# Optimization experiments

Measured on AMD Instinct MI355X. Metric: run time of the kernel, lower is better.

The kernel has to match this reference:

```python
import jax, jax.numpy as jnp
import numpy as np

N_NODES = 100000
N_EDGES = 600000
NODE_IN = 387
HID = 128
EDGE_DIM = 7


def _p(key, shape, scale=0.02):
    return jax.random.normal(key, shape, dtype=jnp.float32) * scale


def setup_inputs() -> dict:
    key = jax.random.key(0)
    ks = jax.random.split(key, 24)
    x = jax.random.normal(ks[0], (N_NODES, NODE_IN), dtype=jnp.float32)
    edge_index = jax.random.randint(ks[1], (2, N_EDGES), 0, N_NODES, dtype=jnp.int64)
    edge_attr = jax.random.normal(ks[2], (N_EDGES, EDGE_DIM), dtype=jnp.float32)
    return {
        "x": x,
        "edge_index": edge_index,
        "edge_attr": edge_attr,
        # conv1: edge lin (7 -> 387), mlp (387 -> 128 -> 128)
        "e1_w": _p(ks[3], (EDGE_DIM, NODE_IN)), "e1_b": jnp.zeros((NODE_IN,), jnp.float32),
        "m1_w1": _p(ks[4], (NODE_IN, HID)), "m1_b1": jnp.zeros((HID,), jnp.float32),
        "m1_w2": _p(ks[5], (HID, HID)), "m1_b2": jnp.zeros((HID,), jnp.float32),
        # conv2: edge lin (7 -> 128), mlp (128 -> 128 -> 128)
        "e2_w": _p(ks[6], (EDGE_DIM, HID)), "e2_b": jnp.zeros((HID,), jnp.float32),
        "m2_w1": _p(ks[7], (HID, HID)), "m2_b1": jnp.zeros((HID,), jnp.float32),
        "m2_w2": _p(ks[8], (HID, HID)), "m2_b2": jnp.zeros((HID,), jnp.float32),
        # edge_mlp: (2*128+7 -> 128 -> 2); dropout is identity at eval
        "em_w1": _p(ks[9], (2 * HID + EDGE_DIM, HID)), "em_b1": jnp.zeros((HID,), jnp.float32),
        "em_w2": _p(ks[10], (HID, 2)), "em_b2": jnp.zeros((2,), jnp.float32),
    }


def gine_conv(x, src, dst, edge_attr, ew, eb, w1, b1, w2, b2, eps=0.0):
    # message: relu(x_j + Lin(edge_attr)); aggregate sum at destination
    msg = jax.nn.relu(x[src] + edge_attr @ ew + eb)  # [E, D]
    aggr = jax.ops.segment_sum(msg, dst, num_segments=x.shape[0])  # [N, D]
    h = (1.0 + eps) * x + aggr
    return jax.nn.relu(h @ w1 + b1) @ w2 + b2


def reference(x, edge_index, edge_attr,
              e1_w, e1_b, m1_w1, m1_b1, m1_w2, m1_b2,
              e2_w, e2_b, m2_w1, m2_b1, m2_w2, m2_b2,
              em_w1, em_b1, em_w2, em_b2):
    src, dst = edge_index[0], edge_index[1]
    h = gine_conv(x, src, dst, edge_attr, e1_w, e1_b, m1_w1, m1_b1, m1_w2, m1_b2)
    h = jax.nn.relu(h)
    h = gine_conv(h, src, dst, edge_attr, e2_w, e2_b, m2_w1, m2_b1, m2_w2, m2_b2)
    h = jax.nn.relu(h)
    edge_input = jnp.concatenate([h[src], h[dst], edge_attr], axis=1)  # [E, 263]
    return jax.nn.relu(edge_input @ em_w1 + em_b1) @ em_w2 + em_b2  # [E, 2]
```

## Files before the change

### kernel.cpp

```cpp
#include <hip/hip_runtime.h>


using f32x4 = __attribute__((ext_vector_type(4))) float;
using s16x8 = __attribute__((ext_vector_type(8))) short;

#define N_NODES 100000
#define N_EDGES 600000
#define NODE_IN 387
#define KPAD    416
#define HID     128
#define NB_SCAN 391

__device__ __forceinline__ unsigned short f2bf(float f) {
    unsigned u = __float_as_uint(f);
    u += 0x7FFFu + ((u >> 16) & 1u);
    return (unsigned short)(u >> 16);
}
__device__ __forceinline__ float bf2f(short h) {
    return __uint_as_float(((unsigned)(unsigned short)h) << 16);
}

__global__ __launch_bounds__(256) void k_decode(const unsigned* __restrict__ w,
                                                int* __restrict__ s32,
                                                int* __restrict__ d32) {
    __shared__ unsigned long long bs[4];
    __shared__ int is64_s;
    const int t = threadIdx.x;
    unsigned any = 0;
    for (int i = 1 + 2 * t; i < 2048; i += 512) any |= w[i];
    unsigned long long b = __ballot(any != 0);
    if ((t & 63) == 0) bs[t >> 6] = b;
    __syncthreads();
    if (t == 0) is64_s = ((bs[0] | bs[1] | bs[2] | bs[3]) == 0ULL) ? 1 : 0;
    __syncthreads();
    const int is64 = is64_s;
    const int e = blockIdx.x * 256 + t;
    if (e < N_EDGES) {
        if (is64) {
            s32[e] = (int)w[2 * e];
            d32[e] = (int)w[2 * N_EDGES + 2 * e];
        } else {
            s32[e] = (int)w[e];
            d32[e] = (int)w[N_EDGES + e];
        }
    }
}

__global__ __launch_bounds__(256) void k_prep(const float* __restrict__ w1,
                                              const float* __restrict__ w2,
                                              const float* __restrict__ v1,
                                              const float* __restrict__ v2,
                                              const float* __restrict__ ew1,
                                              unsigned short* __restrict__ W1t,
                                              unsigned short* __restrict__ W2t,
                                              unsigned short* __restrict__ V1t,
                                              unsigned short* __restrict__ V2t,
                                              unsigned short* __restrict__ EW1t) {
    int i = blockIdx.x * 256 + threadIdx.x;
    if (i < 128 * KPAD) {
        int c = i / KPAD, k = i - c * KPAD;
        W1t[i] = (k < NODE_IN) ? f2bf(w1[k * HID + c]) : (unsigned short)0;
        return;
    }
    i -= 128 * KPAD;
    if (i < 16384) { int c = i >> 7, k = i & 127; W2t[i] = f2bf(w2[k * HID + c]); return; }
    i -= 16384;
    if (i < 16384) { int c = i >> 7, k = i & 127; V1t[i] = f2bf(v1[k * HID + c]); return; }
    i -= 16384;
    if (i < 16384) { int c = i >> 7, k = i & 127; V2t[i] = f2bf(v2[k * HID + c]); return; }
    i -= 16384;
    if (i < 32768) { int c = i >> 8, k = i & 255; EW1t[i] = f2bf(ew1[k * HID + c]); return; }
}

__global__ __launch_bounds__(256) void k_castx(const float* __restrict__ x,
                                               unsigned short* __restrict__ xbf) {
    const int g = blockIdx.x * 256 + threadIdx.x;
    if (g >= N_NODES * 52) return;
    const int row = g / 52, c0 = (g - row * 52) * 8;
    s16x8 v;
#pragma unroll
    for (int j = 0; j < 8; ++j) {
        const int c = c0 + j;
        v[j] = (c < NODE_IN) ? (short)f2bf(x[row * NODE_IN + c]) : (short)0;
    }
    *(s16x8*)&xbf[row * KPAD + c0] = v;
}

__global__ __launch_bounds__(256) void k_hist(const int* __restrict__ d32,
                                              int* __restrict__ cnt) {
    const int e = blockIdx.x * 256 + threadIdx.x;
    if (e < N_EDGES) atomicAdd(&cnt[d32[e]], 1);
}

__global__ __launch_bounds__(256) void k_scanA(const int* __restrict__ cnt,
                                               int* __restrict__ bsum) {
    __shared__ int wt[4];
    const int t = threadIdx.x;
    const int i = blockIdx.x * 256 + t;
    int v = (i < N_NODES) ? cnt[i] : 0;
#pragma unroll
    for (int off = 32; off; off >>= 1) v += __shfl_down(v, off);
    if ((t & 63) == 0) wt[t >> 6] = v;
    __syncthreads();
    if (t == 0) bsum[blockIdx.x] = wt[0] + wt[1] + wt[2] + wt[3];
}

__global__ __launch_bounds__(256) void k_scanC(int* __restrict__ cnt,
                                               const int* __restrict__ bsum) {
    __shared__ int wt[4];
    __shared__ int wt2[4];
    __shared__ int sh_bofs;
    const int t = threadIdx.x, b = blockIdx.x;
    int accp = 0;
    for (int i = t; i < NB_SCAN; i += 256) if (i < b) accp += bsum[i];
#pragma unroll
    for (int off = 32; off; off >>= 1) accp += __shfl_down(accp, off);
    if ((t & 63) == 0) wt[t >> 6] = accp;
    __syncthreads();
    if (t == 0) sh_bofs = wt[0] + wt[1] + wt[2] + wt[3];
    const int i = b * 256 + t;
    const int v = (i < N_NODES) ? cnt[i] : 0;
    int inc = v;
    const int lane = t & 63;
#pragma unroll
    for (int off = 1; off < 64; off <<= 1) {
        int u = __shfl_up(inc, off);
        if (lane >= off) inc += u;
    }
    if (lane == 63) wt2[t >> 6] = inc;
    __syncthreads();
    int wbase = 0;
    for (int wI = 0; wI < (t >> 6); ++wI) wbase += wt2[wI];
    if (i < N_NODES) cnt[i] = sh_bofs + wbase + inc - v;
}

__global__ __launch_bounds__(256) void k_scatter(const int* __restrict__ s32,
                                                 const int* __restrict__ d32,
                                                 const float* __restrict__ ea,
                                                 int* __restrict__ cur,
                                                 int* __restrict__ ss2,
                                                 int* __restrict__ ds2,
                                                 float* __restrict__ eas) {
    const int e = blockIdx.x * 256 + threadIdx.x;
    if (e < N_EDGES) {
        const int d = d32[e];
        const int pos = atomicAdd(&cur[d], 1);
        ss2[pos] = s32[e];
        ds2[pos] = d;
#pragma unroll
        for (int q = 0; q < 7; ++q) eas[pos * 8 + q] = ea[e * 7 + q];
        eas[pos * 8 + 7] = 0.f;
    }
}

#define STAGE_B(dst, srcbase, stride_) do {                                   \
    const int col_ = t >> 1, h_ = t & 1;                                      \
    *(s16x8*)&(dst)[col_ * 40 + h_ * 16] =                                    \
        *(const s16x8*)&(srcbase)[col_ * (stride_) + h_ * 16];                \
    *(s16x8*)&(dst)[col_ * 40 + h_ * 16 + 8] =                                \
        *(const s16x8*)&(srcbase)[col_ * (stride_) + h_ * 16 + 8];            \
} while (0)

__global__ __launch_bounds__(256) void k_edge1(const unsigned short* __restrict__ xbf,
                                               const int* __restrict__ ss2,
                                               const int* __restrict__ ds2,
                                               const float* __restrict__ eas,
                                               const float* __restrict__ e1w,
                                               const float* __restrict__ e1b,
                                               const unsigned short* __restrict__ W1t,
                                               float* __restrict__ yagg) {
    __shared__ __align__(16) char pool[31232];
    unsigned short* Asm = (unsigned short*)(pool);
    unsigned short* Bsm = (unsigned short*)(pool + 5120);
    float* e1w_s = (float*)(pool + 15360);
    float* e1b_s = (float*)(pool + 27008);
    float* ea_s  = (float*)(pool + 28672);
    int* ss_s    = (int*)(pool + 30720);
    int* dst_s   = (int*)(pool + 30976);
    float* Csm   = (float*)(pool);

    const int t = threadIdx.x;
    const int e0 = blockIdx.x * 64;

    if (t < 64) ss_s[t] = ss2[e0 + t];
    else if (t < 128) dst_s[t - 64] = ds2[e0 + (t - 64)];
    for (int i = t; i < 7 * KPAD; i += 256) {
        int q = i / KPAD, k = i - q * KPAD;
        e1w_s[i] = (k < NODE_IN) ? e1w[q * NODE_IN + k] : 0.f;
    }
    for (int i = t; i < KPAD; i += 256) e1b_s[i] = (i < NODE_IN) ? e1b[i] : 0.f;
    for (int i = t; i < 512; i += 256) ea_s[i] = eas[e0 * 8 + i];
    __syncthreads();

    const int lane = t & 63, wid = t >> 6;
    const int wr = wid >> 1, wc = wid & 1;
    const int r = t >> 2, kc = (t & 3) * 8;
    const int srow = ss_s[r];
    float eav[7];
#pragma unroll
    for (int q = 0; q < 7; ++q) eav[q] = ea_s[r * 8 + q];

    f32x4 acc[2][4];
    const f32x4 zero = {0.f, 0.f, 0.f, 0.f};
#pragma unroll
    for (int mi = 0; mi < 2; ++mi)
#pragma unroll
        for (int ni = 0; ni < 4; ++ni) acc[mi][ni] = zero;

    s16x8 xa_n = *(const s16x8*)&xbf[srow * KPAD + kc];
    for (int ks = 0; ks < 13; ++ks) {
        const s16x8 xa = xa_n;
        if (ks < 12) xa_n = *(const s16x8*)&xbf[srow * KPAD + (ks + 1) * 32 + kc];
        {
            const int kb = ks * 32 + kc;
            s16x8 v;
#pragma unroll
            for (int j = 0; j < 8; ++j) {
                const int k = kb + j;
                float le = e1b_s[k];
#pragma unroll
                for (int q = 0; q < 7; ++q) le = fmaf(eav[q], e1w_s[q * KPAD + k], le);
                v[j] = (short)f2bf(fmaxf(bf2f(xa[j]) + le, 0.f));
            }
            *(s16x8*)&Asm[r * 40 + kc] = v;
        }
        STAGE_B(Bsm, &W1t[ks * 32], KPAD);
        __syncthreads();
        const int koff = (lane >> 4) * 8;
        const int rA = lane & 15;
        s16x8 a0 = *(const s16x8*)&Asm[(wr * 32 + rA) * 40 + koff];
        s16x8 a1 = *(const s16x8*)&Asm[(wr * 32 + 16 + rA) * 40 + koff];
#pragma unroll
        for (int ni = 0; ni < 4; ++ni) {
            s16x8 b = *(const s16x8*)&Bsm[(wc * 64 + ni * 16 + rA) * 40 + koff];
            acc[0][ni] = __builtin_amdgcn_mfma_f32_16x16x32_bf16(a0, b, acc[0][ni], 0, 0, 0);
            acc[1][ni] = __builtin_amdgcn_mfma_f32_16x16x32_bf16(a1, b, acc[1][ni], 0, 0, 0);
        }
        __syncthreads();
    }
    const int g = lane >> 4;
    const int cb = wc * 64 + (lane & 15);
#pragma unroll
    for (int p = 0; p < 2; ++p) {
        if (wr == p) {
#pragma unroll
            for (int mi = 0; mi < 2; ++mi)
#pragma unroll
                for (int reg = 0; reg < 4; ++reg) {
                    const int row = mi * 16 + g * 4 + reg;
#pragma unroll
                    for (int ni = 0; ni < 4; ++ni)
                        Csm[row * 129 + cb + ni * 16] = acc[mi][ni][reg];
                }
        }
        __syncthreads();
        if (t < 128) {
            const int base = p * 32;
            float s = 0.f;
            int prev = dst_s[base];
            for (int rr = 0; rr < 32; ++rr) {
                const int d = dst_s[base + rr];
                const float v = Csm[rr * 129 + t];
                if (d != prev) { atomicAdd(&yagg[prev * HID + t], s); s = 0.f; prev = d; }
                s += v;
            }
            atomicAdd(&yagg[prev * HID + t], s);
        }
        __syncthreads();
    }
}

__global__ __launch_bounds__(256) void k_node1(const unsigned short* __restrict__ xbf,
                                               const float* __restrict__ yagg,
                                               const unsigned short* __restrict__ W1t,
                                               const unsigned short* __restrict__ W2t,
                                               const float* __restrict__ b1,
                                               const float* __restrict__ b2,
                                               unsigned short* __restrict__ r1b) {
    __shared__ __align__(16) unsigned short Asm[64 * 40];
    __shared__ __align__(16) unsigned short Bsm[128 * 40];
    __shared__ __align__(16) unsigned short Hsm[64 * 136];
    const int t = threadIdx.x;
    const int i0 = blockIdx.x * 64;
    const int lane = t & 63, wid = t >> 6, wr = wid >> 1, wc = wid & 1;
    const int r = t >> 2, kc = (t & 3) * 8;
    const int rg = i0 + r;
    const bool rvalid = rg < N_NODES;

    f32x4 acc[2][4];
    const f32x4 zero = {0.f, 0.f, 0.f, 0.f};
#pragma unroll
    for (int mi = 0; mi < 2; ++mi)
#pragma unroll
        for (int ni = 0; ni < 4; ++ni) acc[mi][ni] = zero;

    for (int ks = 0; ks < 13; ++ks) {
        {
            s16x8 v;
            if (rvalid) v = *(const s16x8*)&xbf[rg * KPAD + ks * 32 + kc];
            else {
#pragma unroll
                for (int j = 0; j < 8; ++j) v[j] = 0;
            }
            *(s16x8*)&Asm[r * 40 + kc] = v;
        }
        STAGE_B(Bsm, &W1t[ks * 32], KPAD);
        __syncthreads();
        const int koff = (lane >> 4) * 8;
        const int rA = lane & 15;
        s16x8 a0 = *(const s16x8*)&Asm[(wr * 32 + rA) * 40 + koff];
        s16x8 a1 = *(const s16x8*)&Asm[(wr * 32 + 16 + rA) * 40 + koff];
#pragma unroll
        for (int ni = 0; ni < 4; ++ni) {
            s16x8 b = *(const s16x8*)&Bsm[(wc * 64 + ni * 16 + rA) * 40 + koff];
            acc[0][ni] = __builtin_amdgcn_mfma_f32_16x16x32_bf16(a0, b, acc[0][ni], 0, 0, 0);
            acc[1][ni] = __builtin_amdgcn_mfma_f32_16x16x32_bf16(a1, b, acc[1][ni], 0, 0, 0);
        }
        __syncthreads();
    }
    const int jb = wc * 64 + (lane & 15);
#pragma unroll
    for (int mi = 0; mi < 2; ++mi) {
#pragma unroll
        for (int reg = 0; reg < 4; ++reg) {
            const int rloc = wr * 32 + mi * 16 + (lane >> 4) * 4 + reg;
            const int rowg = i0 + rloc;
#pragma unroll
            for (int ni = 0; ni < 4; ++ni) {
                const int j = jb + ni * 16;
                float v = acc[mi][ni][reg];
                if (rowg < N_NODES) {
                    v += yagg[rowg * HID + j] + b1[j];
                    v = fmaxf(v, 0.f);
                } else v = 0.f;
                Hsm[rloc * 136 + j] = f2bf(v);
            }
        }
    }
    __syncthreads();
    f32x4 acc2[2][4];
#pragma unroll
    for (int mi = 0; mi < 2; ++mi)
#pragma unroll
        for (int ni = 0; ni < 4; ++ni) acc2[mi][ni] = zero;

    for (int ks = 0; ks < 4; ++ks) {
        STAGE_B(Bsm, &W2t[ks * 32], HID);
        __syncthreads();
        const int koff = (lane >> 4) * 8;
        const int rA = lane & 15;
        s16x8 a0 = *(const s16x8*)&Hsm[(wr * 32 + rA) * 136 + ks * 32 + koff];
        s16x8 a1 = *(const s16x8*)&Hsm[(wr * 32 + 16 + rA) * 136 + ks * 32 + koff];
#pragma unroll
        for (int ni = 0; ni < 4; ++ni) {
            s16x8 b = *(const s16x8*)&Bsm[(wc * 64 + ni * 16 + rA) * 40 + koff];
            acc2[0][ni] = __builtin_amdgcn_mfma_f32_16x16x32_bf16(a0, b, acc2[0][ni], 0, 0, 0);
            acc2[1][ni] = __builtin_amdgcn_mfma_f32_16x16x32_bf16(a1, b, acc2[1][ni], 0, 0, 0);
        }
        __syncthreads();
    }
#pragma unroll
    for (int mi = 0; mi < 2; ++mi) {
#pragma unroll
        for (int reg = 0; reg < 4; ++reg) {
            const int rloc = wr * 32 + mi * 16 + (lane >> 4) * 4 + reg;
            const int rowg = i0 + rloc;
            if (rowg < N_NODES) {
#pragma unroll
                for (int ni = 0; ni < 4; ++ni) {
                    const int j = jb + ni * 16;
                    float v = acc2[mi][ni][reg] + b2[j];
                    r1b[rowg * HID + j] = f2bf(fmaxf(v, 0.f));
                }
            }
        }
    }
}

__global__ __launch_bounds__(256) void k_edge2(const unsigned short* __restrict__ r1b,
                                               const int* __restrict__ ss2,
                                               const int* __restrict__ ds2,
                                               const float* __restrict__ eas,
                                               const float* __restrict__ e2w,
                                               const float* __restrict__ e2b,
                                               float* __restrict__ agg2) {
    __shared__ float w_s[7 * HID];
    __shared__ float b_s[HID];
    __shared__ float Csm[64 * 129];
    __shared__ float ea_s[64 * 8];
    __shared__ int ss_s[64];
    __shared__ int ds_s[64];
    const int t = threadIdx.x;
    const int e0 = blockIdx.x * 64;
    for (int i = t; i < 7 * HID; i += 256) w_s[i] = e2w[i];
    if (t < HID) b_s[t] = e2b[t];
    if (t < 64) ss_s[t] = ss2[e0 + t];
    else if (t < 128) ds_s[t - 64] = ds2[e0 + (t - 64)];
    for (int i = t; i < 512; i += 256) ea_s[i] = eas[e0 * 8 + i];
    __syncthreads();

    const int r = t >> 2, c0 = (t & 3) * 32;
    const int s = ss_s[r];
    float eav[7];
#pragma unroll
    for (int q = 0; q < 7; ++q) eav[q] = ea_s[r * 8 + q];
    const s16x8* rp = (const s16x8*)&r1b[s * HID + c0];
#pragma unroll
    for (int u = 0; u < 4; ++u) {
        s16x8 hv = rp[u];
#pragma unroll
        for (int j = 0; j < 8; ++j) {
            const int c = c0 + u * 8 + j;
            float v = bf2f(hv[j]) + b_s[c];
#pragma unroll
            for (int q = 0; q < 7; ++q) v = fmaf(eav[q], w_s[q * HID + c], v);
            Csm[r * 129 + c] = fmaxf(v, 0.f);
        }
    }
    __syncthreads();
    if (t < 128) {
        float ssum = 0.f;
        int prev = ds_s[0];
        for (int rr = 0; rr < 64; ++rr) {
            const int d = ds_s[rr];
            const float v = Csm[rr * 129 + t];
            if (d != prev) { atomicAdd(&agg2[prev * HID + t], ssum); ssum = 0.f; prev = d; }
            ssum += v;
        }
        atomicAdd(&agg2[prev * HID + t], ssum);
    }
}

__global__ __launch_bounds__(256) void k_node2(const unsigned short* __restrict__ r1b,
                                               const float* __restrict__ agg2,
                                               const unsigned short* __restrict__ V1t,
                                               const unsigned short* __restrict__ V2t,
                                               const float* __restrict__ b1,
                                               const float* __restrict__ b2,
                                               unsigned short* __restrict__ r2) {
    __shared__ __align__(16) unsigned short Asm[64 * 40];
    __shared__ __align__(16) unsigned short Bsm[128 * 40];
    __shared__ __align__(16) unsigned short Hsm[64 * 136];
    const int t = threadIdx.x;
    const int i0 = blockIdx.x * 64;
    const int lane = t & 63, wid = t >> 6, wr = wid >> 1, wc = wid & 1;
    const int r = t >> 2, kc = (t & 3) * 8;
    const int rg = i0 + r;
    const bool rvalid = rg < N_NODES;

    f32x4 acc[2][4];
    const f32x4 zero = {0.f, 0.f, 0.f, 0.f};
#pragma unroll
    for (int mi = 0; mi < 2; ++mi)
#pragma unroll
        for (int ni = 0; ni < 4; ++ni) acc[mi][ni] = zero;

    for (int ks = 0; ks < 4; ++ks) {
        {
            const int kb = ks * 32 + kc;
            s16x8 v;
            if (rvalid) {
                const s16x8 ra = *(const s16x8*)&r1b[rg * HID + kb];
                const f32x4* pb = (const f32x4*)&agg2[rg * HID + kb];
                f32x4 w0 = pb[0], w1 = pb[1];
#pragma unroll
                for (int j = 0; j < 4; ++j) v[j] = (short)f2bf(bf2f(ra[j]) + w0[j]);
#pragma unroll
                for (int j = 0; j < 4; ++j) v[4 + j] = (short)f2bf(bf2f(ra[4 + j]) + w1[j]);
            } else {
#pragma unroll
                for (int j = 0; j < 8; ++j) v[j] = 0;
            }
            *(s16x8*)&Asm[r * 40 + kc] = v;
        }
        STAGE_B(Bsm, &V1t[ks * 32], HID);
        __syncthreads();
        const int koff = (lane >> 4) * 8;
        const int rA = lane & 15;
        s16x8 a0 = *(const s16x8*)&Asm[(wr * 32 + rA) * 40 + koff];
        s16x8 a1 = *(const s16x8*)&Asm[(wr * 32 + 16 + rA) * 40 + koff];
#pragma unroll
        for (int ni = 0; ni < 4; ++ni) {
            s16x8 b = *(const s16x8*)&Bsm[(wc * 64 + ni * 16 + rA) * 40 + koff];
            acc[0][ni] = __builtin_amdgcn_mfma_f32_16x16x32_bf16(a0, b, acc[0][ni], 0, 0, 0);
            acc[1][ni] = __builtin_amdgcn_mfma_f32_16x16x32_bf16(a1, b, acc[1][ni], 0, 0, 0);
        }
        __syncthreads();
    }
    const int jb = wc * 64 + (lane & 15);
#pragma unroll
    for (int mi = 0; mi < 2; ++mi) {
#pragma unroll
        for (int reg = 0; reg < 4; ++reg) {
            const int rloc = wr * 32 + mi * 16 + (lane >> 4) * 4 + reg;
            const int rowg = i0 + rloc;
#pragma unroll
            for (int ni = 0; ni < 4; ++ni) {
                const int j = jb + ni * 16;
                float v = acc[mi][ni][reg];
                if (rowg < N_NODES) {
                    v += b1[j];
                    v = fmaxf(v, 0.f);
                } else v = 0.f;
                Hsm[rloc * 136 + j] = f2bf(v);
            }
        }
    }
    __syncthreads();
    f32x4 acc2[2][4];
#pragma unroll
    for (int mi = 0; mi < 2; ++mi)
#pragma unroll
        for (int ni = 0; ni < 4; ++ni) acc2[mi][ni] = zero;

    for (int ks = 0; ks < 4; ++ks) {
        STAGE_B(Bsm, &V2t[ks * 32], HID);
        __syncthreads();
        const int koff = (lane >> 4) * 8;
        const int rA = lane & 15;
        s16x8 a0 = *(const s16x8*)&Hsm[(wr * 32 + rA) * 136 + ks * 32 + koff];
        s16x8 a1 = *(const s16x8*)&Hsm[(wr * 32 + 16 + rA) * 136 + ks * 32 + koff];
#pragma unroll
        for (int ni = 0; ni < 4; ++ni) {
            s16x8 b = *(const s16x8*)&Bsm[(wc * 64 + ni * 16 + rA) * 40 + koff];
            acc2[0][ni] = __builtin_amdgcn_mfma_f32_16x16x32_bf16(a0, b, acc2[0][ni], 0, 0, 0);
            acc2[1][ni] = __builtin_amdgcn_mfma_f32_16x16x32_bf16(a1, b, acc2[1][ni], 0, 0, 0);
        }
        __syncthreads();
    }
#pragma unroll
    for (int mi = 0; mi < 2; ++mi) {
#pragma unroll
        for (int reg = 0; reg < 4; ++reg) {
            const int rloc = wr * 32 + mi * 16 + (lane >> 4) * 4 + reg;
            const int rowg = i0 + rloc;
            if (rowg < N_NODES) {
#pragma unroll
                for (int ni = 0; ni < 4; ++ni) {
                    const int j = jb + ni * 16;
                    float v = acc2[mi][ni][reg] + b2[j];
                    r2[rowg * HID + j] = f2bf(fmaxf(v, 0.f));
                }
            }
        }
    }
}

__global__ __launch_bounds__(256) void k_head(const unsigned short* __restrict__ r2,
                                              const int* __restrict__ srcp,
                                              const int* __restrict__ dstp,
                                              const float* __restrict__ ea,
                                              const unsigned short* __restrict__ EW1t,
                                              const float* __restrict__ emw1,
                                              const float* __restrict__ emb1,
                                              const float* __restrict__ emw2,
                                              const float* __restrict__ emb2,
                                              float* __restrict__ out) {
    __shared__ __align__(16) unsigned short Asm[64 * 40];
    __shared__ __align__(16) unsigned short Bsm[128 * 40];
    __shared__ float Hsm[64 * 129];
    __shared__ float ew_ea[7 * HID];
    __shared__ float eb1_s[HID];
    __shared__ float w2_s[256];
    __shared__ float b2_s[2];
    __shared__ float ea_s[64 * 8];
    __shared__ int src_s[64];
    __shared__ int dst_s[64];
    __shared__ float red[512];
    const int t = threadIdx.x;
    const int e0 = blockIdx.x * 64;

    for (int i = t; i < 7 * HID; i += 256) ew_ea[i] = emw1[256 * HID + i];
    if (t < HID) eb1_s[t] = emb1[t];
    if (t < 256) w2_s[t] = emw2[t];
    if (t < 2) b2_s[t] = emb2[t];
    for (int i = t; i < 64 * 7; i += 256) {
        int r = i / 7, q = i - r * 7;
        ea_s[r * 8 + q] = ea[(e0 + r) * 7 + q];
    }
    if (t < 64) src_s[t] = srcp[e0 + t];
    else if (t < 128) dst_s[t - 64] = dstp[e0 + (t - 64)];
    __syncthreads();

    const int lane = t & 63, wid = t >> 6, wr = wid >> 1, wc = wid & 1;
    const int r = t >> 2, kc = (t & 3) * 8;

    f32x4 acc[2][4];
    const f32x4 zero = {0.f, 0.f, 0.f, 0.f};
#pragma unroll
    for (int mi = 0; mi < 2; ++mi)
#pragma unroll
        for (int ni = 0; ni < 4; ++ni) acc[mi][ni] = zero;

    for (int ks = 0; ks < 8; ++ks) {
        {
            const int k = ks * 32 + kc;
            const unsigned short* p = (k < HID) ? &r2[src_s[r] * HID + k]
                                                : &r2[dst_s[r] * HID + (k - HID)];
            *(s16x8*)&Asm[r * 40 + kc] = *(const s16x8*)p;
        }
        STAGE_B(Bsm, &EW1t[ks * 32], 256);
        __syncthreads();
        const int koff = (lane >> 4) * 8;
        const int rA = lane & 15;
        s16x8 a0 = *(const s16x8*)&Asm[(wr * 32 + rA) * 40 + koff];
        s16x8 a1 = *(const s16x8*)&Asm[(wr * 32 + 16 + rA) * 40 + koff];
#pragma unroll
        for (int ni = 0; ni < 4; ++ni) {
            s16x8 b = *(const s16x8*)&Bsm[(wc * 64 + ni * 16 + rA) * 40 + koff];
            acc[0][ni] = __builtin_amdgcn_mfma_f32_16x16x32_bf16(a0, b, acc[0][ni], 0, 0, 0);
            acc[1][ni] = __builtin_amdgcn_mfma_f32_16x16x32_bf16(a1, b, acc[1][ni], 0, 0, 0);
        }
        __syncthreads();
    }
    const int jb = wc * 64 + (lane & 15);
#pragma unroll
    for (int mi = 0; mi < 2; ++mi) {
#pragma unroll
        for (int reg = 0; reg < 4; ++reg) {
            const int rloc = wr * 32 + mi * 16 + (lane >> 4) * 4 + reg;
#pragma unroll
            for (int ni = 0; ni < 4; ++ni) {
                const int j = jb + ni * 16;
                float v = acc[mi][ni][reg] + eb1_s[j];
#pragma unroll
                for (int q = 0; q < 7; ++q)
                    v = fmaf(ea_s[rloc * 8 + q], ew_ea[q * HID + j], v);
                Hsm[rloc * 129 + j] = fmaxf(v, 0.f);
            }
        }
    }
    __syncthreads();
    {
        const int e = t & 63, p = t >> 6;
        const float* hb = &Hsm[e * 129 + p * 32];
        float s0 = 0.f, s1 = 0.f;
#pragma unroll
        for (int j = 0; j < 32; ++j) {
            const float h = hb[j];
            s0 = fmaf(h, w2_s[(p * 32 + j) * 2], s0);
            s1 = fmaf(h, w2_s[(p * 32 + j) * 2 + 1], s1);
        }
        red[(e * 4 + p) * 2] = s0;
        red[(e * 4 + p) * 2 + 1] = s1;
    }
    __syncthreads();
    if (t < 64) {
        float o0 = b2_s[0], o1 = b2_s[1];
#pragma unroll
        for (int p = 0; p < 4; ++p) {
            o0 += red[(t * 4 + p) * 2];
            o1 += red[(t * 4 + p) * 2 + 1];
        }
        out[(e0 + t) * 2] = o0;
        out[(e0 + t) * 2 + 1] = o1;
    }
}

extern "C" void kernel_launch(void* const* d_in, const int* in_sizes, int n_in,
                              void* d_out, int out_size, void* d_ws, size_t ws_size,
                              hipStream_t stream) {
    (void)in_sizes; (void)n_in; (void)out_size; (void)ws_size;
    const float* x    = (const float*)d_in[0];
    const unsigned* eidx = (const unsigned*)d_in[1];
    const float* ea   = (const float*)d_in[2];
    const float* e1w  = (const float*)d_in[3];
    const float* e1b  = (const float*)d_in[4];
    const float* m1w1 = (const float*)d_in[5];
    const float* m1b1 = (const float*)d_in[6];
    const float* m1w2 = (const float*)d_in[7];
    const float* m1b2 = (const float*)d_in[8];
    const float* e2w  = (const float*)d_in[9];
    const float* e2b  = (const float*)d_in[10];
    const float* m2w1 = (const float*)d_in[11];
    const float* m2b1 = (const float*)d_in[12];
    const float* m2w2 = (const float*)d_in[13];
    const float* m2b2 = (const float*)d_in[14];
    const float* emw1 = (const float*)d_in[15];
    const float* emb1 = (const float*)d_in[16];
    const float* emw2 = (const float*)d_in[17];
    const float* emb2 = (const float*)d_in[18];
    float* out = (float*)d_out;

    char* ws = (char*)d_ws;
    float* yagg = (float*)(ws + 0);
    unsigned short* r1b = (unsigned short*)(ws + 51200000);
    unsigned short* r2  = (unsigned short*)(ws + 76800000);
    float* eas          = (float*)(ws + 76800000);
    unsigned short* xbf = (unsigned short*)(ws + 102400000);
    unsigned short* W1t  = (unsigned short*)(ws + 185600000);
    unsigned short* W2t  = (unsigned short*)(ws + 185706496);
    unsigned short* V1t  = (unsigned short*)(ws + 185739264);
    unsigned short* V2t  = (unsigned short*)(ws + 185772032);
    unsigned short* EW1t = (unsigned short*)(ws + 185804800);
    int* s32  = (int*)(ws + 185870336);
    int* d32  = (int*)(ws + 188270336);
    int* ss2  = (int*)(ws + 190670336);
    int* ds2  = (int*)(ws + 193070336);
    int* cnt  = (int*)(ws + 195470336);
    int* bsum = (int*)(ws + 195870336);

    hipMemsetAsync(yagg, 0, (size_t)N_NODES * HID * 4, stream);
    hipMemsetAsync(cnt, 0, (size_t)N_NODES * 4, stream);
    k_decode<<<2344, 256, 0, stream>>>(eidx, s32, d32);
    k_prep<<<528, 256, 0, stream>>>(m1w1, m1w2, m2w1, m2w2, emw1, W1t, W2t, V1t, V2t, EW1t);
    k_castx<<<(N_NODES * 52 + 255) / 256, 256, 0, stream>>>(x, xbf);
    k_hist<<<2344, 256, 0, stream>>>(d32, cnt);
    k_scanA<<<NB_SCAN, 256, 0, stream>>>(cnt, bsum);
    k_scanC<<<NB_SCAN, 256, 0, stream>>>(cnt, bsum);
    k_scatter<<<2344, 256, 0, stream>>>(s32, d32, ea, cnt, ss2, ds2, eas);
    k_edge1<<<N_EDGES / 64, 256, 0, stream>>>(xbf, ss2, ds2, eas, e1w, e1b, W1t, yagg);
    k_node1<<<(N_NODES + 63) / 64, 256, 0, stream>>>(xbf, yagg, W1t, W2t, m1b1, m1b2, r1b);
    hipMemsetAsync(yagg, 0, (size_t)N_NODES * HID * 4, stream);
    k_edge2<<<N_EDGES / 64, 256, 0, stream>>>(r1b, ss2, ds2, eas, e2w, e2b, yagg);
    k_node2<<<(N_NODES + 63) / 64, 256, 0, stream>>>(r1b, yagg, V1t, V2t, m2b1, m2b2, r2);
    k_head<<<N_EDGES / 64, 256, 0, stream>>>(r2, s32, d32, ea, EW1t, emw1, emb1, emw2, emb2, out);
}
```

Measured before the change: 1.076 ms.

## Fuse conv2 edge aggregation into node MLP via CSR gather; MFMA edge-linear in conv1

Replaces conv2's atomic scatter edge kernel, memset and separate node kernel with one kernel. It gathers each node's incoming edges through a CSR rowptr built during the scan, then runs the node MLP. In conv1, the per-element 7-term edge-linear FMA loop becomes a small bf16 MFMA against a prepacked weight/bias matrix, and the segmented atomics are split across all 256 threads. The head now reads edges in dst-sorted order and writes outputs through a stored permutation. This removes atomics and a 51MB memset at the cost of load imbalance from per-node serial edge loops and extra syncs and bf16 rounding in edge1.

Result: no change. 1.079 ms (+0.3%).

```diff
diff --git a/kernel.cpp b/kernel.cpp
--- a/kernel.cpp
+++ b/kernel.cpp
@@ -51,11 +51,14 @@
                                               const float* __restrict__ v1,
                                               const float* __restrict__ v2,
                                               const float* __restrict__ ew1,
+                                              const float* __restrict__ e1w,
+                                              const float* __restrict__ e1b,
                                               unsigned short* __restrict__ W1t,
                                               unsigned short* __restrict__ W2t,
                                               unsigned short* __restrict__ V1t,
                                               unsigned short* __restrict__ V2t,
-                                              unsigned short* __restrict__ EW1t) {
+                                              unsigned short* __restrict__ EW1t,
+                                              unsigned short* __restrict__ E1T) {
     int i = blockIdx.x * 256 + threadIdx.x;
     if (i < 128 * KPAD) {
         int c = i / KPAD, k = i - c * KPAD;
@@ -70,6 +73,17 @@
     if (i < 16384) { int c = i >> 7, k = i & 127; V2t[i] = f2bf(v2[k * HID + c]); return; }
     i -= 16384;
     if (i < 32768) { int c = i >> 8, k = i & 255; EW1t[i] = f2bf(ew1[k * HID + c]); return; }
+    i -= 32768;
+    if (i < 416 * 32) {
+        int f = i >> 5, q = i & 31;
+        unsigned short v = 0;
+        if (f < NODE_IN) {
+            if (q < 7) v = f2bf(e1w[q * NODE_IN + f]);
+            else if (q == 7) v = f2bf(e1b[f]);
+        }
+        E1T[i] = v;
+        return;
+    }
 }
 
 __global__ __launch_bounds__(256) void k_castx(const float* __restrict__ x,
@@ -106,7 +120,8 @@
 }
 
 __global__ __launch_bounds__(256) void k_scanC(int* __restrict__ cnt,
-                                               const int* __restrict__ bsum) {
+                                               const int* __restrict__ bsum,
+                                               int* __restrict__ rowptr) {
     __shared__ int wt[4];
     __shared__ int wt2[4];
     __shared__ int sh_bofs;
@@ -131,7 +146,11 @@
     __syncthreads();
     int wbase = 0;
     for (int wI = 0; wI < (t >> 6); ++wI) wbase += wt2[wI];
-    if (i < N_NODES) cnt[i] = sh_bofs + wbase + inc - v;
+    if (i < N_NODES) {
+        const int ex = sh_bofs + wbase + inc - v;
+        cnt[i] = ex;
+        rowptr[i] = ex;
+    }
 }
 
 __global__ __launch_bounds__(256) void k_scatter(const int* __restrict__ s32,
@@ -140,6 +159,7 @@
                                                  int* __restrict__ cur,
                                                  int* __restrict__ ss2,
                                                  int* __restrict__ ds2,
+                                                 int* __restrict__ ep,
                                                  float* __restrict__ eas) {
     const int e = blockIdx.x * 256 + threadIdx.x;
     if (e < N_EDGES) {
@@ -147,6 +167,7 @@
         const int pos = atomicAdd(&cur[d], 1);
         ss2[pos] = s32[e];
         ds2[pos] = d;
+        ep[pos]  = e;
 #pragma unroll
         for (int q = 0; q < 7; ++q) eas[pos * 8 + q] = ea[e * 7 + q];
         eas[pos * 8 + 7] = 0.f;
@@ -165,41 +186,47 @@
                                                const int* __restrict__ ss2,
                                                const int* __restrict__ ds2,
                                                const float* __restrict__ eas,
-                                               const float* __restrict__ e1w,
-                                               const float* __restrict__ e1b,
+                                               const unsigned short* __restrict__ E1T,
                                                const unsigned short* __restrict__ W1t,
                                                float* __restrict__ yagg) {
-    __shared__ __align__(16) char pool[31232];
-    unsigned short* Asm = (unsigned short*)(pool);
-    unsigned short* Bsm = (unsigned short*)(pool + 5120);
-    float* e1w_s = (float*)(pool + 15360);
-    float* e1b_s = (float*)(pool + 27008);
-    float* ea_s  = (float*)(pool + 28672);
-    int* ss_s    = (int*)(pool + 30720);
-    int* dst_s   = (int*)(pool + 30976);
-    float* Csm   = (float*)(pool);
+    __shared__ __align__(16) char pool[26880];
+    unsigned short* Asm  = (unsigned short*)(pool);
+    unsigned short* Bsm  = (unsigned short*)(pool + 5120);
+    unsigned short* Bsm2 = (unsigned short*)(pool + 15360);
+    float* le_lds = (float*)(pool + 17920);
+    int* ss_s     = (int*)(pool + 26368);
+    int* dst_s    = (int*)(pool + 26624);
+    float* Csm    = (float*)(pool);
 
     const int t = threadIdx.x;
     const int e0 = blockIdx.x * 64;
 
     if (t < 64) ss_s[t] = ss2[e0 + t];
     else if (t < 128) dst_s[t - 64] = ds2[e0 + (t - 64)];
-    for (int i = t; i < 7 * KPAD; i += 256) {
-        int q = i / KPAD, k = i - q * KPAD;
-        e1w_s[i] = (k < NODE_IN) ? e1w[q * NODE_IN + k] : 0.f;
-    }
-    for (int i = t; i < KPAD; i += 256) e1b_s[i] = (i < NODE_IN) ? e1b[i] : 0.f;
-    for (int i = t; i < 512; i += 256) ea_s[i] = eas[e0 * 8 + i];
-    __syncthreads();
 
     const int lane = t & 63, wid = t >> 6;
     const int wr = wid >> 1, wc = wid & 1;
     const int r = t >> 2, kc = (t & 3) * 8;
+    const int rA = lane & 15;
+    const int koff = (lane >> 4) * 8;
+
+    {
+        s16x8 v;
+#pragma unroll
+        for (int j = 0; j < 8; ++j) v[j] = 0;
+        if (kc == 0) {
+#pragma unroll
+            for (int q = 0; q < 7; ++q) v[q] = (short)f2bf(eas[(e0 + r) * 8 + q]);
+            v[7] = (short)0x3F80;
+        }
+        *(s16x8*)&Asm[r * 40 + kc] = v;
+    }
+    __syncthreads();
+    const s16x8 eap0 = *(const s16x8*)&Asm[(wr * 32 + rA) * 40 + koff];
+    const s16x8 eap1 = *(const s16x8*)&Asm[(wr * 32 + 16 + rA) * 40 + koff];
+    __syncthreads();
+
     const int srow = ss_s[r];
-    float eav[7];
-#pragma unroll
-    for (int q = 0; q < 7; ++q) eav[q] = ea_s[r * 8 + q];
-
     f32x4 acc[2][4];
     const f32x4 zero = {0.f, 0.f, 0.f, 0.f};
 #pragma unroll
@@ -211,23 +238,34 @@
     for (int ks = 0; ks < 13; ++ks) {
         const s16x8 xa = xa_n;
         if (ks < 12) xa_n = *(const s16x8*)&xbf[srow * KPAD + (ks + 1) * 32 + kc];
+        STAGE_B(Bsm, &W1t[ks * 32], KPAD);
+        if (t < 128) {
+            const int n = t >> 2, qg = (t & 3) * 8;
+            *(s16x8*)&Bsm2[n * 40 + qg] = *(const s16x8*)&E1T[(ks * 32 + n) * 32 + qg];
+        }
+        __syncthreads();
         {
-            const int kb = ks * 32 + kc;
+            s16x8 b2 = *(const s16x8*)&Bsm2[(wc * 16 + rA) * 40 + koff];
+            f32x4 le0 = __builtin_amdgcn_mfma_f32_16x16x32_bf16(eap0, b2, zero, 0, 0, 0);
+            f32x4 le1 = __builtin_amdgcn_mfma_f32_16x16x32_bf16(eap1, b2, zero, 0, 0, 0);
+            const int cw = wc * 16 + rA;
+#pragma unroll
+            for (int reg = 0; reg < 4; ++reg) {
+                const int row = wr * 32 + (lane >> 4) * 4 + reg;
+                le_lds[row * 33 + cw] = le0[reg];
+                le_lds[(row + 16) * 33 + cw] = le1[reg];
+            }
+        }
+        __syncthreads();
+        {
+            const float* lep = &le_lds[r * 33 + kc];
             s16x8 v;
 #pragma unroll
-            for (int j = 0; j < 8; ++j) {
-                const int k = kb + j;
-                float le = e1b_s[k];
-#pragma unroll
-                for (int q = 0; q < 7; ++q) le = fmaf(eav[q], e1w_s[q * KPAD + k], le);
-                v[j] = (short)f2bf(fmaxf(bf2f(xa[j]) + le, 0.f));
-            }
+            for (int j = 0; j < 8; ++j)
+                v[j] = (short)f2bf(fmaxf(bf2f(xa[j]) + lep[j], 0.f));
             *(s16x8*)&Asm[r * 40 + kc] = v;
         }
-        STAGE_B(Bsm, &W1t[ks * 32], KPAD);
-        __syncthreads();
-        const int koff = (lane >> 4) * 8;
-        const int rA = lane & 15;
+        __syncthreads();
         s16x8 a0 = *(const s16x8*)&Asm[(wr * 32 + rA) * 40 + koff];
         s16x8 a1 = *(const s16x8*)&Asm[(wr * 32 + 16 + rA) * 40 + koff];
 #pragma unroll
@@ -238,8 +276,8 @@
         }
         __syncthreads();
     }
-    const int g = lane >> 4;
-    const int cb = wc * 64 + (lane & 15);
+    const int gq = lane >> 4;
+    const int cb = wc * 64 + rA;
 #pragma unroll
     for (int p = 0; p < 2; ++p) {
         if (wr == p) {
@@ -247,24 +285,25 @@
             for (int mi = 0; mi < 2; ++mi)
 #pragma unroll
                 for (int reg = 0; reg < 4; ++reg) {
-                    const int row = mi * 16 + g * 4 + reg;
+                    const int row = mi * 16 + gq * 4 + reg;
 #pragma unroll
                     for (int ni = 0; ni < 4; ++ni)
                         Csm[row * 129 + cb + ni * 16] = acc[mi][ni][reg];
                 }
         }
         __syncthreads();
-        if (t < 128) {
-            const int base = p * 32;
+        {
+            const int col = t & 127, half = t >> 7;
+            const int b0 = p * 32 + half * 16;
             float s = 0.f;
-            int prev = dst_s[base];
-            for (int rr = 0; rr < 32; ++rr) {
-                const int d = dst_s[base + rr];
-                const float v = Csm[rr * 129 + t];
-                if (d != prev) { atomicAdd(&yagg[prev * HID + t], s); s = 0.f; prev = d; }
+            int prev = dst_s[b0];
+            for (int rr = 0; rr < 16; ++rr) {
+                const int d = dst_s[b0 + rr];
+                const float v = Csm[(half * 16 + rr) * 129 + col];
+                if (d != prev) { atomicAdd(&yagg[prev * HID + col], s); s = 0.f; prev = d; }
                 s += v;
             }
-            atomicAdd(&yagg[prev * HID + t], s);
+            atomicAdd(&yagg[prev * HID + col], s);
         }
         __syncthreads();
     }
@@ -377,108 +416,100 @@
     }
 }
 
-__global__ __launch_bounds__(256) void k_edge2(const unsigned short* __restrict__ r1b,
+__global__ __launch_bounds__(256) void k_conv2(const unsigned short* __restrict__ r1b,
                                                const int* __restrict__ ss2,
-                                               const int* __restrict__ ds2,
                                                const float* __restrict__ eas,
+                                               const int* __restrict__ rowptr,
                                                const float* __restrict__ e2w,
                                                const float* __restrict__ e2b,
-                                               float* __restrict__ agg2) {
-    __shared__ float w_s[7 * HID];
-    __shared__ float b_s[HID];
-    __shared__ float Csm[64 * 129];
-    __shared__ float ea_s[64 * 8];
-    __shared__ int ss_s[64];
-    __shared__ int ds_s[64];
-    const int t = threadIdx.x;
-    const int e0 = blockIdx.x * 64;
-    for (int i = t; i < 7 * HID; i += 256) w_s[i] = e2w[i];
-    if (t < HID) b_s[t] = e2b[t];
-    if (t < 64) ss_s[t] = ss2[e0 + t];
-    else if (t < 128) ds_s[t - 64] = ds2[e0 + (t - 64)];
-    for (int i = t; i < 512; i += 256) ea_s[i] = eas[e0 * 8 + i];
-    __syncthreads();
-
-    const int r = t >> 2, c0 = (t & 3) * 32;
-    const int s = ss_s[r];
-    float eav[7];
-#pragma unroll
-    for (int q = 0; q < 7; ++q) eav[q] = ea_s[r * 8 + q];
-    const s16x8* rp = (const s16x8*)&r1b[s * HID + c0];
-#pragma unroll
-    for (int u = 0; u < 4; ++u) {
-        s16x8 hv = rp[u];
-#pragma unroll
-        for (int j = 0; j < 8; ++j) {
-            const int c = c0 + u * 8 + j;
-            float v = bf2f(hv[j]) + b_s[c];
-#pragma unroll
-            for (int q = 0; q < 7; ++q) v = fmaf(eav[q], w_s[q * HID + c], v);
-            Csm[r * 129 + c] = fmaxf(v, 0.f);
-        }
-    }
-    __syncthreads();
-    if (t < 128) {
-        float ssum = 0.f;
-        int prev = ds_s[0];
-        for (int rr = 0; rr < 64; ++rr) {
-            const int d = ds_s[rr];
-            const float v = Csm[rr * 129 + t];
-            if (d != prev) { atomicAdd(&agg2[prev * HID + t], ssum); ssum = 0.f; prev = d; }
-            ssum += v;
-        }
-        atomicAdd(&agg2[prev * HID + t], ssum);
-    }
-}
-
-__global__ __launch_bounds__(256) void k_node2(const unsigned short* __restrict__ r1b,
-                                               const float* __restrict__ agg2,
                                                const unsigned short* __restrict__ V1t,
                                                const unsigned short* __restrict__ V2t,
                                                const float* __restrict__ b1,
                                                const float* __restrict__ b2,
                                                unsigned short* __restrict__ r2) {
-    __shared__ __align__(16) unsigned short Asm[64 * 40];
+    __shared__ float w_s[7 * HID];
+    __shared__ float eb_s[HID];
     __shared__ __align__(16) unsigned short Bsm[128 * 40];
     __shared__ __align__(16) unsigned short Hsm[64 * 136];
     const int t = threadIdx.x;
     const int i0 = blockIdx.x * 64;
+    for (int i = t; i < 7 * HID; i += 256) w_s[i] = e2w[i];
+    if (t < HID) eb_s[t] = e2b[t];
+    __syncthreads();
+
+    const int r = t >> 2, c0 = (t & 3) * 32;
+    const int g = i0 + r;
+    float acc32[32];
+#pragma unroll
+    for (int j = 0; j < 32; ++j) acc32[j] = 0.f;
+
+    if (g < N_NODES) {
+        const int eB = rowptr[g];
+        const int eE = (g + 1 < N_NODES) ? rowptr[g + 1] : N_EDGES;
+        for (int e = eB; e < eE; ++e) {
+            float eav[7];
+#pragma unroll
+            for (int q = 0; q < 7; ++q) eav[q] = eas[e * 8 + q];
+            const int src = ss2[e];
+            const s16x8* rp = (const s16x8*)&r1b[src * HID + c0];
+#pragma unroll
+            for (int u = 0; u < 4; ++u) {
+                s16x8 hv = rp[u];
+                float vv[8];
+#pragma unroll
+                for (int j = 0; j < 8; ++j) vv[j] = bf2f(hv[j]) + eb_s[c0 + u * 8 + j];
+#pragma unroll
+                for (int q = 0; q < 7; ++q) {
+                    const f32x4 w0 = *(const f32x4*)&w_s[q * HID + c0 + u * 8];
+                    const f32x4 w1 = *(const f32x4*)&w_s[q * HID + c0 + u * 8 + 4];
+#pragma unroll
+                    for (int j = 0; j < 4; ++j) {
+                        vv[j]     = fmaf(eav[q], w0[j], vv[j]);
+                        vv[4 + j] = fmaf(eav[q], w1[j], vv[4 + j]);
+                    }
+                }
+#pragma unroll
+                for (int j = 0; j < 8; ++j) acc32[u * 8 + j] += fmaxf(vv[j], 0.f);
+            }
+        }
+    }
+    {
+        if (g < N_NODES) {
+            const s16x8* rp = (const s16x8*)&r1b[g * HID + c0];
+#pragma unroll
+            for (int u = 0; u < 4; ++u) {
+                s16x8 hv = rp[u];
+                s16x8 o;
+#pragma unroll
+                for (int j = 0; j < 8; ++j)
+                    o[j] = (short)f2bf(bf2f(hv[j]) + acc32[u * 8 + j]);
+                *(s16x8*)&Hsm[r * 136 + c0 + u * 8] = o;
+            }
+        } else {
+            s16x8 o;
+#pragma unroll
+            for (int j = 0; j < 8; ++j) o[j] = 0;
+#pragma unroll
+            for (int u = 0; u < 4; ++u)
+                *(s16x8*)&Hsm[r * 136 + c0 + u * 8] = o;
+        }
+    }
+    __syncthreads();
+
     const int lane = t & 63, wid = t >> 6, wr = wid >> 1, wc = wid & 1;
-    const int r = t >> 2, kc = (t & 3) * 8;
-    const int rg = i0 + r;
-    const bool rvalid = rg < N_NODES;
-
+    const int rA = lane & 15, koff = (lane >> 4) * 8;
+    const f32x4 zero = {0.f, 0.f, 0.f, 0.f};
     f32x4 acc[2][4];
-    const f32x4 zero = {0.f, 0.f, 0.f, 0.f};
 #pragma unroll
     for (int mi = 0; mi < 2; ++mi)
 #pragma unroll
         for (int ni = 0; ni < 4; ++ni) acc[mi][ni] = zero;
 
     for (int ks = 0; ks < 4; ++ks) {
-        {
-            const int kb = ks * 32 + kc;
-            s16x8 v;
-            if (rvalid) {
-                const s16x8 ra = *(const s16x8*)&r1b[rg * HID + kb];
-                const f32x4* pb = (const f32x4*)&agg2[rg * HID + kb];
-                f32x4 w0 = pb[0], w1 = pb[1];
-#pragma unroll
-                for (int j = 0; j < 4; ++j) v[j] = (short)f2bf(bf2f(ra[j]) + w0[j]);
-#pragma unroll
-                for (int j = 0; j < 4; ++j) v[4 + j] = (short)f2bf(bf2f(ra[4 + j]) + w1[j]);
-            } else {
-#pragma unroll
-                for (int j = 0; j < 8; ++j) v[j] = 0;
-            }
-            *(s16x8*)&Asm[r * 40 + kc] = v;
-        }
         STAGE_B(Bsm, &V1t[ks * 32], HID);
         __syncthreads();
-        const int koff = (lane >> 4) * 8;
-        const int rA = lane & 15;
-        s16x8 a0 = *(const s16x8*)&Asm[(wr * 32 + rA) * 40 + koff];
-        s16x8 a1 = *(const s16x8*)&Asm[(wr * 32 + 16 + rA) * 40 + koff];
+        s16x8 a0 = *(const s16x8*)&Hsm[(wr * 32 + rA) * 136 + ks * 32 + koff];
+        s16x8 a1 = *(const s16x8*)&Hsm[(wr * 32 + 16 + rA) * 136 + ks * 32 + koff];
 #pragma unroll
         for (int ni = 0; ni < 4; ++ni) {
             s16x8 b = *(const s16x8*)&Bsm[(wc * 64 + ni * 16 + rA) * 40 + koff];
@@ -487,22 +518,17 @@
         }
         __syncthreads();
     }
-    const int jb = wc * 64 + (lane & 15);
+    const int jb = wc * 64 + rA;
 #pragma unroll
     for (int mi = 0; mi < 2; ++mi) {
 #pragma unroll
         for (int reg = 0; reg < 4; ++reg) {
             const int rloc = wr * 32 + mi * 16 + (lane >> 4) * 4 + reg;
-            const int rowg = i0 + rloc;
 #pragma unroll
             for (int ni = 0; ni < 4; ++ni) {
                 const int j = jb + ni * 16;
-                float v = acc[mi][ni][reg];
-                if (rowg < N_NODES) {
-                    v += b1[j];
-                    v = fmaxf(v, 0.f);
-                } else v = 0.f;
-                Hsm[rloc * 136 + j] = f2bf(v);
+                float v = acc[mi][ni][reg] + b1[j];
+                Hsm[rloc * 136 + j] = f2bf(fmaxf(v, 0.f));
             }
         }
     }
@@ -516,8 +542,6 @@
     for (int ks = 0; ks < 4; ++ks) {
         STAGE_B(Bsm, &V2t[ks * 32], HID);
         __syncthreads();
-        const int koff = (lane >> 4) * 8;
-        const int rA = lane & 15;
         s16x8 a0 = *(const s16x8*)&Hsm[(wr * 32 + rA) * 136 + ks * 32 + koff];
         s16x8 a1 = *(const s16x8*)&Hsm[(wr * 32 + 16 + rA) * 136 + ks * 32 + koff];
 #pragma unroll
@@ -547,9 +571,10 @@
 }
 
 __global__ __launch_bounds__(256) void k_head(const unsigned short* __restrict__ r2,
-                                              const int* __restrict__ srcp,
-                                              const int* __restrict__ dstp,
-                                              const float* __restrict__ ea,
+                                              const int* __restrict__ ss2,
+                                              const int* __restrict__ ds2,
+                                              const int* __restrict__ ep,
+                                              const float* __restrict__ eas,
                                               const unsigned short* __restrict__ EW1t,
                                               const float* __restrict__ emw1,
                                               const float* __restrict__ emb1,
@@ -566,6 +591,7 @@
     __shared__ float ea_s[64 * 8];
     __shared__ int src_s[64];
     __shared__ int dst_s[64];
+    __shared__ int ep_s[64];
     __shared__ float red[512];
     const int t = threadIdx.x;
     const int e0 = blockIdx.x * 64;
@@ -574,12 +600,10 @@
     if (t < HID) eb1_s[t] = emb1[t];
     if (t < 256) w2_s[t] = emw2[t];
     if (t < 2) b2_s[t] = emb2[t];
-    for (int i = t; i < 64 * 7; i += 256) {
-        int r = i / 7, q = i - r * 7;
-        ea_s[r * 8 + q] = ea[(e0 + r) * 7 + q];
-    }
-    if (t < 64) src_s[t] = srcp[e0 + t];
-    else if (t < 128) dst_s[t - 64] = dstp[e0 + (t - 64)];
+    for (int i = t; i < 512; i += 256) ea_s[i] = eas[e0 * 8 + i];
+    if (t < 64) src_s[t] = ss2[e0 + t];
+    else if (t < 128) dst_s[t - 64] = ds2[e0 + (t - 64)];
+    else if (t < 192) ep_s[t - 128] = ep[e0 + (t - 128)];
     __syncthreads();
 
     const int lane = t & 63, wid = t >> 6, wr = wid >> 1, wc = wid & 1;
@@ -652,8 +676,9 @@
             o0 += red[(t * 4 + p) * 2];
             o1 += red[(t * 4 + p) * 2 + 1];
         }
-        out[(e0 + t) * 2] = o0;
-        out[(e0 + t) * 2 + 1] = o1;
+        const int oe = ep_s[t];
+        out[oe * 2] = o0;
+        out[oe * 2 + 1] = o1;
     }
 }
 
@@ -684,35 +709,39 @@
 
     char* ws = (char*)d_ws;
     float* yagg = (float*)(ws + 0);
+    unsigned short* r2 = (unsigned short*)(ws + 0);
     unsigned short* r1b = (unsigned short*)(ws + 51200000);
-    unsigned short* r2  = (unsigned short*)(ws + 76800000);
     float* eas          = (float*)(ws + 76800000);
-    unsigned short* xbf = (unsigned short*)(ws + 102400000);
-    unsigned short* W1t  = (unsigned short*)(ws + 185600000);
-    unsigned short* W2t  = (unsigned short*)(ws + 185706496);
-    unsigned short* V1t  = (unsigned short*)(ws + 185739264);
-    unsigned short* V2t  = (unsigned short*)(ws + 185772032);
-    unsigned short* EW1t = (unsigned short*)(ws + 185804800);
-    int* s32  = (int*)(ws + 185870336);
-    int* d32  = (int*)(ws + 188270336);
-    int* ss2  = (int*)(ws + 190670336);
-    int* ds2  = (int*)(ws + 193070336);
-    int* cnt  = (int*)(ws + 195470336);
-    int* bsum = (int*)(ws + 195870336);
+    unsigned short* xbf = (unsigned short*)(ws + 96000000);
+    unsigned short* W1t  = (unsigned short*)(ws + 179200000);
+    unsigned short* W2t  = (unsigned short*)(ws + 179306496);
+    unsigned short* V1t  = (unsigned short*)(ws + 179339264);
+    unsigned short* V2t  = (unsigned short*)(ws + 179372032);
+    unsigned short* EW1t = (unsigned short*)(ws + 179404800);
+    unsigned short* E1T  = (unsigned short*)(ws + 179470336);
+    int* s32    = (int*)(ws + 179496960);
+    int* d32    = (int*)(ws + 181896960);
+    int* ss2    = (int*)(ws + 184296960);
+    int* ds2    = (int*)(ws + 186696960);
+    int* ep     = (int*)(ws + 189096960);
+    int* cnt    = (int*)(ws + 191496960);
+    int* rowptr = (int*)(ws + 191896960);
+    int* bsum   = (int*)(ws + 192296960);
 
     hipMemsetAsync(yagg, 0, (size_t)N_NODES * HID * 4, stream);
     hipMemsetAsync(cnt, 0, (size_t)N_NODES * 4, stream);
     k_decode<<<2344, 256, 0, stream>>>(eidx, s32, d32);
-    k_prep<<<528, 256, 0, stream>>>(m1w1, m1w2, m2w1, m2w2, emw1, W1t, W2t, V1t, V2t, EW1t);
+    k_prep<<<580, 256, 0, stream>>>(m1w1, m1w2, m2w1, m2w2, emw1, e1w, e1b,
+                                    W1t, W2t, V1t, V2t, EW1t, E1T);
     k_castx<<<(N_NODES * 52 + 255) / 256, 256, 0, stream>>>(x, xbf);
     k_hist<<<2344, 256, 0, stream>>>(d32, cnt);
     k_scanA<<<NB_SCAN, 256, 0, stream>>>(cnt, bsum);
-    k_scanC<<<NB_SCAN, 256, 0, stream>>>(cnt, bsum);
-    k_scatter<<<2344, 256, 0, stream>>>(s32, d32, ea, cnt, ss2, ds2, eas);
-    k_edge1<<<N_EDGES / 64, 256, 0, stream>>>(xbf, ss2, ds2, eas, e1w, e1b, W1t, yagg);
+    k_scanC<<<NB_SCAN, 256, 0, stream>>>(cnt, bsum, rowptr);
+    k_scatter<<<2344, 256, 0, stream>>>(s32, d32, ea, cnt, ss2, ds2, ep, eas);
+    k_edge1<<<N_EDGES / 64, 256, 0, stream>>>(xbf, ss2, ds2, eas, E1T, W1t, yagg);
     k_node1<<<(N_NODES + 63) / 64, 256, 0, stream>>>(xbf, yagg, W1t, W2t, m1b1, m1b2, r1b);
-    hipMemsetAsync(yagg, 0, (size_t)N_NODES * HID * 4, stream);
-    k_edge2<<<N_EDGES / 64, 256, 0, stream>>>(r1b, ss2, ds2, eas, e2w, e2b, yagg);
-    k_node2<<<(N_NODES + 63) / 64, 256, 0, stream>>>(r1b, yagg, V1t, V2t, m2b1, m2b2, r2);
-    k_head<<<N_EDGES / 64, 256, 0, stream>>>(r2, s32, d32, ea, EW1t, emw1, emb1, emw2, emb2, out);
-}
+    k_conv2<<<(N_NODES + 63) / 64, 256, 0, stream>>>(r1b, ss2, eas, rowptr, e2w, e2b,
+                                                     V1t, V2t, m2b1, m2b2, r2);
+    k_head<<<N_EDGES / 64, 256, 0, stream>>>(r2, ss2, ds2, ep, eas, EW1t,
+                                             emw1, emb1, emw2, emb2, out);
+}
```
